# Optimization experiments

Measured on AMD Instinct MI355X. Metric: run time of the kernel, lower is better.

The kernel has to match this reference:

```python
import jax, jax.numpy as jnp
import numpy as np
from jax import lax

B, C, W, H = 4, 64, 128, 128
K = 9            # snake kernel length
OC = 64          # out channels
EXTEND_SCOPE = 1.0
EPS = 1e-5
DN = ('NCHW', 'OIHW', 'NCHW')


def setup_inputs() -> dict:
    key = jax.random.key(0)
    ks = jax.random.split(key, 4)
    f = jax.random.normal(ks[0], (B, C, W, H), jnp.float32)
    offset_w = jax.random.normal(ks[1], (2 * K, C, 3, 3), jnp.float32) * 0.05
    offset_b = jnp.zeros((2 * K,), jnp.float32)
    bn_gamma = jnp.ones((2 * K,), jnp.float32)
    bn_beta = jnp.zeros((2 * K,), jnp.float32)
    bn_mean = jnp.zeros((2 * K,), jnp.float32)
    bn_var = jnp.ones((2 * K,), jnp.float32)
    conv_w = jax.random.normal(ks[2], (OC, C, K, 1), jnp.float32) * 0.05
    conv_b = jnp.zeros((OC,), jnp.float32)
    gn_gamma = jnp.ones((OC,), jnp.float32)
    gn_beta = jnp.zeros((OC,), jnp.float32)
    return dict(f=f, offset_w=offset_w, offset_b=offset_b, bn_gamma=bn_gamma,
                bn_beta=bn_beta, bn_mean=bn_mean, bn_var=bn_var,
                conv_w=conv_w, conv_b=conv_b, gn_gamma=gn_gamma, gn_beta=gn_beta)


def _dsconv(f, offset_w, offset_b, bn_gamma, bn_beta, bn_mean, bn_var,
            conv_w, conv_b, gn_gamma, gn_beta):
    # 1) offset branch: 3x3 conv -> BN (eval) -> tanh
    off = lax.conv_general_dilated(f, offset_w, (1, 1), 'SAME', dimension_numbers=DN)
    off = off + offset_b[None, :, None, None]
    off = (off - bn_mean[None, :, None, None]) * lax.rsqrt(bn_var + EPS)[None, :, None, None]
    off = off * bn_gamma[None, :, None, None] + bn_beta[None, :, None, None]
    off = jnp.tanh(off)
    y_off = off[:, :K]                      # [B,K,W,H]  (morph==0 uses y offsets)

    # 2) cumulative offset recurrence outward from the kernel center.
    # NOTE: indices 0 and K-1 keep their raw (non-accumulated) offsets,
    # exactly reproducing the original loop `for i in range(1, center)`.
    c = K // 2
    offs = [y_off[:, k] for k in range(K)]  # each [B,W,H]
    new = list(offs)
    new[c] = jnp.zeros_like(offs[c])
    for i in range(1, c):
        new[c + i] = new[c + i - 1] + offs[c + i]
        new[c - i] = new[c - i + 1] + offs[c - i]
    y_cum = jnp.stack(new, axis=1)          # [B,K,W,H]

    # 3) sampling coordinates (morph==0): y = row index + accumulated offset,
    # x = col index + linspace(-K//2, K//2, K) (python floor-div semantics).
    lin = jnp.linspace((-K) // 2, K // 2, K).astype(f.dtype)      # [-5..4] for K=9
    y = jnp.arange(W, dtype=f.dtype)[None, None, :, None] + y_cum * EXTEND_SCOPE
    x = jnp.broadcast_to(jnp.arange(H, dtype=f.dtype)[None, None, None, :]
                         + lin[None, :, None, None], (B, K, W, H))
    # layout [B, K*W, H] with row index = w*K + k
    ys = jnp.transpose(y, (0, 2, 1, 3)).reshape(B, K * W, H)
    xs = jnp.transpose(x, (0, 2, 1, 3)).reshape(B, K * W, H)

    # 4) bilinear gather from f (NCHW -> BWHC for channel-last gathers)
    y0 = jnp.clip(jnp.floor(ys).astype(jnp.int32), 0, W - 1)
    y1 = jnp.clip(y0 + 1, 0, W - 1)
    x0 = jnp.clip(jnp.floor(xs).astype(jnp.int32), 0, H - 1)
    x1 = jnp.clip(x0 + 1, 0, H - 1)
    fb = jnp.transpose(f, (0, 2, 3, 1))                  # [B,W,H,C]
    gather = jax.vmap(lambda fm, yy, xx: fm[yy, xx])     # -> [B,K*W,H,C]
    va0 = gather(fb, y0, x0)
    va1 = gather(fb, y0, x1)
    vb0 = gather(fb, y1, x0)
    vb1 = gather(fb, y1, x1)
    y0f, y1f = y0.astype(f.dtype), y1.astype(f.dtype)
    x0f, x1f = x0.astype(f.dtype), x1.astype(f.dtype)
    out = (va0 * ((y1f - ys) * (x1f - xs))[..., None]
           + va1 * ((y1f - ys) * (xs - x0f))[..., None]
           + vb0 * ((ys - y0f) * (x1f - xs))[..., None]
           + vb1 * ((ys - y0f) * (xs - x0f))[..., None])
    deformed = jnp.transpose(out, (0, 3, 1, 2))          # [B,C,K*W,H]

    # 5) (K,1)-strided conv collapses the K snake samples -> [B,OC,W,H]
    z = lax.conv_general_dilated(deformed, conv_w, (K, 1), 'VALID', dimension_numbers=DN)
    z = z + conv_b[None, :, None, None]

    # 6) GroupNorm(OC//4 groups) + ReLU
    G = OC // 4
    zg = z.reshape(B, G, OC // G, W, H)
    mu = zg.mean(axis=(2, 3, 4), keepdims=True)
    var = zg.var(axis=(2, 3, 4), keepdims=True)
    zg = (zg - mu) * lax.rsqrt(var + EPS)
    z = zg.reshape(B, OC, W, H) * gn_gamma[None, :, None, None] + gn_beta[None, :, None, None]
    return jax.nn.relu(z)


def reference(f, offset_w, offset_b, bn_gamma, bn_beta, bn_mean, bn_var,
              conv_w, conv_b, gn_gamma, gn_beta):
    return _dsconv(f, offset_w, offset_b, bn_gamma, bn_beta, bn_mean, bn_var,
                   conv_w, conv_b, gn_gamma, gn_beta)
```

## Files before the change

kernel.cpp:

```cpp
#include <hip/hip_runtime.h>
#include <hip/hip_bf16.h>

#define EPSV 1e-5f

typedef __attribute__((ext_vector_type(8))) short short8;
typedef __attribute__((ext_vector_type(4))) float f32x4;

__global__ __launch_bounds__(256) void k_transpose(const float* __restrict__ f,
                                                   ushort* __restrict__ fbh) {
    int blk = blockIdx.x;
    int xt  = blk & 1;
    int y   = (blk >> 1) & 127;
    int b   = blk >> 8;
    __shared__ float tile[64][65];
    int t  = threadIdx.x;
    int x  = t & 63;
    int c0 = t >> 6;
    const float* src = f + (((size_t)b * 64) * 128 + y) * 128 + xt * 64;
#pragma unroll
    for (int i = 0; i < 64; i += 4) {
        tile[c0 + i][x] = src[(size_t)(c0 + i) * (128 * 128) + x];
    }
    __syncthreads();
    ushort* dst = fbh + (((size_t)b * 128 + y) * 128 + xt * 64) * 64;
    int cc = t & 63;
    int x0 = t >> 6;
#pragma unroll
    for (int i = 0; i < 64; i += 4) {
        dst[(size_t)(x0 + i) * 64 + cc] =
            __bfloat16_as_ushort(__float2bfloat16(tile[cc][x0 + i]));
    }
}

__global__ __launch_bounds__(256) void k_prep(const float* __restrict__ cw,
                                              ushort* __restrict__ wpk,
                                              float* __restrict__ stats) {
    int idx = blockIdx.x * 256 + threadIdx.x;
    int j  = idx & 7;
    int l  = (idx >> 3) & 63;
    int ot = (idx >> 9) & 3;
    int kk = (idx >> 11) & 1;
    int k  = idx >> 12;
    int c  = kk * 32 + ((l >> 4) << 3) + j;
    int oc = (ot << 4) + (l & 15);
    float v = cw[((size_t)oc * 64 + c) * 9 + k];
    wpk[idx] = __bfloat16_as_ushort(__float2bfloat16(v));
    if (idx < 128) stats[idx] = 0.f;
}

__global__ __launch_bounds__(128) void k_off1(const float* __restrict__ f,
                                              const float* __restrict__ ow,
                                              float* __restrict__ offp) {
    int blk = blockIdx.x;
    int cq = blk & 3;
    int w  = (blk >> 2) & 127;
    int b  = blk >> 9;
    int c0 = cq << 4;
    __shared__ float wl[9 * 16 * 12];
    int t = threadIdx.x;
    for (int i = t; i < 9 * 16 * 9; i += 128) {
        int kc  = i / 9;
        int tap = i - kc * 9;
        int k   = kc >> 4;
        int ci  = kc & 15;
        wl[kc * 12 + tap] = ow[((size_t)(k * 64 + c0 + ci)) * 9 + tap];
    }
    __syncthreads();
    int h = t;
    float acc[9];
#pragma unroll
    for (int k = 0; k < 9; ++k) acc[k] = 0.f;
    const float* fbase = f + (((size_t)b * 64 + c0) << 14);
    for (int ci = 0; ci < 16; ++ci) {
        const float* fc = fbase + ((size_t)ci << 14);
        float v[9];
#pragma unroll
        for (int dy = 0; dy < 3; ++dy) {
            int yy = w + dy - 1;
            bool yok = (unsigned)yy < 128u;
#pragma unroll
            for (int dx = 0; dx < 3; ++dx) {
                int xx = h + dx - 1;
                v[dy * 3 + dx] = (yok && ((unsigned)xx < 128u)) ? fc[(yy << 7) + xx] : 0.f;
            }
        }
#pragma unroll
        for (int k = 0; k < 9; ++k) {
            const float* wp = &wl[(k * 16 + ci) * 12];
            float4 wa = *(const float4*)wp;
            float4 wb = *(const float4*)(wp + 4);
            acc[k] += v[0] * wa.x + v[1] * wa.y + v[2] * wa.z + v[3] * wa.w
                    + v[4] * wb.x + v[5] * wb.y + v[6] * wb.z + v[7] * wb.w
                    + v[8] * wp[8];
        }
    }
#pragma unroll
    for (int k = 0; k < 9; ++k)
        offp[(((size_t)cq * 36 + b * 9 + k) << 14) + (w << 7) + h] = acc[k];
}

__global__ __launch_bounds__(256) void k_off2(const float* __restrict__ offp,
                                              const float* __restrict__ ob,
                                              const float* __restrict__ bng,
                                              const float* __restrict__ bnb,
                                              const float* __restrict__ bnm,
                                              const float* __restrict__ bnv,
                                              float* __restrict__ yc) {
    int idx = blockIdx.x * 256 + threadIdx.x;
    int b = idx >> 14;
    int rest = idx & 16383;
    int w = rest >> 7;
    float tk[9];
#pragma unroll
    for (int k = 0; k < 9; ++k) {
        int o = ((b * 9 + k) << 14) + rest;
        float zz = offp[o] + offp[o + 589824] + offp[o + 2 * 589824] + offp[o + 3 * 589824];
        zz += ob[k];
        zz = (zz - bnm[k]) * rsqrtf(bnv[k] + EPSV);
        zz = zz * bng[k] + bnb[k];
        tk[k] = tanhf(zz);
    }
    float nw_[9];
    nw_[4] = 0.f;
    nw_[5] = tk[5];
    nw_[6] = nw_[5] + tk[6];
    nw_[7] = nw_[6] + tk[7];
    nw_[8] = tk[8];
    nw_[3] = tk[3];
    nw_[2] = nw_[3] + tk[2];
    nw_[1] = nw_[2] + tk[1];
    nw_[0] = tk[0];
#pragma unroll
    for (int k = 0; k < 9; ++k)
        yc[((b * 9 + k) << 14) + rest] = (float)w + nw_[k];
}

__global__ __launch_bounds__(256) void k_main(
    const ushort* __restrict__ fbh, const float* __restrict__ yc,
    const ushort* __restrict__ wpk, const float* __restrict__ cb,
    float* __restrict__ z, float* __restrict__ stats)
{
    __shared__ union {
        struct {
            ushort A[32 * 64];
            float  tup[9][32][8];
        } p;
        float Z2[32 * 65];
    } sm;
    __shared__ float redS[16];
    __shared__ float redQ[16];

    int jb = blockIdx.x;
    int orig = (jb & 7) * 256 + (jb >> 3);
    int hq = orig & 3;
    int w  = (orig >> 2) & 127;
    int b  = orig >> 9;
    int t    = threadIdx.x;
    int lane = t & 63;
    int wid  = t >> 6;
    int m = wid & 1;
    int n = wid >> 1;

    for (int i = t; i < 288; i += 256) {
        int k  = i >> 5;
        int px = i & 31;
        int h  = (hq << 5) + px;
        float ys = yc[((b * 9 + k) << 14) + (w << 7) + h];
        float xs = (float)h + (-5.0f + 1.125f * (float)k);
        int y0 = min(max((int)floorf(ys), 0), 127);
        int y1 = min(y0 + 1, 127);
        int x0 = min(max((int)floorf(xs), 0), 127);
        int x1 = min(x0 + 1, 127);
        float wy0 = (float)y1 - ys, wy1 = ys - (float)y0;
        float wx0 = (float)x1 - xs, wx1 = xs - (float)x0;
        float* tp = sm.p.tup[k][px];
        tp[0] = __int_as_float(((((b << 7) + y0) << 7) + x0) << 7);
        tp[1] = __int_as_float(((((b << 7) + y0) << 7) + x1) << 7);
        tp[2] = __int_as_float(((((b << 7) + y1) << 7) + x0) << 7);
        tp[3] = __int_as_float(((((b << 7) + y1) << 7) + x1) << 7);
        tp[4] = wy0 * wx0;
        tp[5] = wy0 * wx1;
        tp[6] = wy1 * wx0;
        tp[7] = wy1 * wx1;
    }
    __syncthreads();

    f32x4 acc0 = {0.f, 0.f, 0.f, 0.f};
    f32x4 acc1 = {0.f, 0.f, 0.f, 0.f};
    const char* fp = (const char*)fbh;
    char* Ab = (char*)sm.p.A;
    int cg = t & 15;
    int pq = t >> 4;
    int cgo = cg << 3;
    const short8* wp8 = (const short8*)wpk;

    for (int k = 0; k < 9; ++k) {
        int fb0 = ((k * 2) * 4 + (n << 1)) * 64 + lane;
        short8 wf00 = wp8[fb0];
        short8 wf01 = wp8[fb0 + 64];
        short8 wf10 = wp8[fb0 + 256];
        short8 wf11 = wp8[fb0 + 320];

#pragma unroll
        for (int s = 0; s < 2; ++s) {
            int px = pq + (s << 4);
            const float* tp = sm.p.tup[k][px];
            float4 tr = *(const float4*)tp;
            float4 tw = *(const float4*)(tp + 4);
            uint2 u00 = *(const uint2*)(fp + __float_as_int(tr.x) + cgo);
            uint2 u01 = *(const uint2*)(fp + __float_as_int(tr.y) + cgo);
            uint2 u10 = *(const uint2*)(fp + __float_as_int(tr.z) + cgo);
            uint2 u11 = *(const uint2*)(fp + __float_as_int(tr.w) + cgo);
            float a0 = __uint_as_float(u00.x << 16) * tw.x + __uint_as_float(u01.x << 16) * tw.y
                     + __uint_as_float(u10.x << 16) * tw.z + __uint_as_float(u11.x << 16) * tw.w;
            float a1 = __uint_as_float(u00.x & 0xffff0000u) * tw.x + __uint_as_float(u01.x & 0xffff0000u) * tw.y
                     + __uint_as_float(u10.x & 0xffff0000u) * tw.z + __uint_as_float(u11.x & 0xffff0000u) * tw.w;
            float a2 = __uint_as_float(u00.y << 16) * tw.x + __uint_as_float(u01.y << 16) * tw.y
                     + __uint_as_float(u10.y << 16) * tw.z + __uint_as_float(u11.y << 16) * tw.w;
            float a3 = __uint_as_float(u00.y & 0xffff0000u) * tw.x + __uint_as_float(u01.y & 0xffff0000u) * tw.y
                     + __uint_as_float(u10.y & 0xffff0000u) * tw.z + __uint_as_float(u11.y & 0xffff0000u) * tw.w;
            uint2 pk;
            pk.x = (uint)__bfloat16_as_ushort(__float2bfloat16(a0))
                 | ((uint)__bfloat16_as_ushort(__float2bfloat16(a1)) << 16);
            pk.y = (uint)__bfloat16_as_ushort(__float2bfloat16(a2))
                 | ((uint)__bfloat16_as_ushort(__float2bfloat16(a3)) << 16);
            int wb = (px << 7) + (cgo ^ ((px & 7) << 4));
            *(uint2*)(Ab + wb) = pk;
        }
        __syncthreads();

        {
            int row = (m << 4) + (lane & 15);
            int rb0 = (row << 7) + ((((lane >> 4) << 4)) ^ ((lane & 7) << 4));
            short8 af0 = *(const short8*)(Ab + rb0);
            short8 af1 = *(const short8*)(Ab + (rb0 ^ 64));
            acc0 = __builtin_amdgcn_mfma_f32_16x16x32_bf16(af0, wf00, acc0, 0, 0, 0);
            acc0 = __builtin_amdgcn_mfma_f32_16x16x32_bf16(af1, wf10, acc0, 0, 0, 0);
            acc1 = __builtin_amdgcn_mfma_f32_16x16x32_bf16(af0, wf01, acc1, 0, 0, 0);
            acc1 = __builtin_amdgcn_mfma_f32_16x16x32_bf16(af1, wf11, acc1, 0, 0, 0);
        }
        __syncthreads();
    }

    int lane15 = lane & 15;
    float b0 = cb[(n << 5) + lane15];
    float b1 = cb[(n << 5) + 16 + lane15];
    float v00 = acc0.x + b0, v01 = acc0.y + b0, v02 = acc0.z + b0, v03 = acc0.w + b0;
    float v10 = acc1.x + b1, v11 = acc1.y + b1, v12 = acc1.z + b1, v13 = acc1.w + b1;
    float s0 = v00 + v01 + v02 + v03;
    float q0 = v00 * v00 + v01 * v01 + v02 * v02 + v03 * v03;
    float s1 = v10 + v11 + v12 + v13;
    float q1 = v10 * v10 + v11 * v11 + v12 * v12 + v13 * v13;
    if (t < 16) { redS[t] = 0.f; redQ[t] = 0.f; }
    __syncthreads();
    int g0 = (n << 3) + (lane15 >> 2);
    atomicAdd(&redS[g0], s0);     atomicAdd(&redQ[g0], q0);
    atomicAdd(&redS[g0 + 4], s1); atomicAdd(&redQ[g0 + 4], q1);
    int pxb = (m << 4) + ((lane >> 4) << 2);
    int ocb = (n << 5) + lane15;
    sm.Z2[(pxb + 0) * 65 + ocb] = v00;
    sm.Z2[(pxb + 1) * 65 + ocb] = v01;
    sm.Z2[(pxb + 2) * 65 + ocb] = v02;
    sm.Z2[(pxb + 3) * 65 + ocb] = v03;
    sm.Z2[(pxb + 0) * 65 + ocb + 16] = v10;
    sm.Z2[(pxb + 1) * 65 + ocb + 16] = v11;
    sm.Z2[(pxb + 2) * 65 + ocb + 16] = v12;
    sm.Z2[(pxb + 3) * 65 + ocb + 16] = v13;
    __syncthreads();
    if (t < 16) {
        atomicAdd(&stats[((size_t)b * 16 + t) * 2 + 0], redS[t]);
        atomicAdd(&stats[((size_t)b * 16 + t) * 2 + 1], redQ[t]);
    }
    int oc = t >> 2, part = t & 3;
    float4 o0, o1;
    o0.x = sm.Z2[(part * 8 + 0) * 65 + oc];
    o0.y = sm.Z2[(part * 8 + 1) * 65 + oc];
    o0.z = sm.Z2[(part * 8 + 2) * 65 + oc];
    o0.w = sm.Z2[(part * 8 + 3) * 65 + oc];
    o1.x = sm.Z2[(part * 8 + 4) * 65 + oc];
    o1.y = sm.Z2[(part * 8 + 5) * 65 + oc];
    o1.z = sm.Z2[(part * 8 + 6) * 65 + oc];
    o1.w = sm.Z2[(part * 8 + 7) * 65 + oc];
    float* zp = z + (((size_t)(b << 6) + oc) << 14) + (w << 7) + (hq << 5) + part * 8;
    *(float4*)zp = o0;
    *(float4*)(zp + 4) = o1;
}

__global__ __launch_bounds__(256) void k_gn(const float* __restrict__ z,
                                            const float* __restrict__ stats,
                                            const float* __restrict__ gg,
                                            const float* __restrict__ gb,
                                            float* __restrict__ out) {
    int idx = blockIdx.x * 256 + threadIdx.x;
    size_t base = (size_t)idx * 4;
    int oc = (int)((base >> 14) & 63);
    int b  = (int)(base >> 20);
    int g  = oc >> 2;
    float sm = stats[((size_t)b * 16 + g) * 2 + 0];
    float sq = stats[((size_t)b * 16 + g) * 2 + 1];
    const float cnt = 65536.f;
    float mu  = sm / cnt;
    float var = sq / cnt - mu * mu;
    float inv = rsqrtf(var + EPSV);
    float gam = gg[oc] * inv;
    float bet = gb[oc] - mu * gam;
    float4 v = *(const float4*)(z + base);
    v.x = fmaxf(v.x * gam + bet, 0.f);
    v.y = fmaxf(v.y * gam + bet, 0.f);
    v.z = fmaxf(v.z * gam + bet, 0.f);
    v.w = fmaxf(v.w * gam + bet, 0.f);
    *(float4*)(out + base) = v;
}

extern "C" void kernel_launch(void* const* d_in, const int* in_sizes, int n_in,
                              void* d_out, int out_size, void* d_ws, size_t ws_size,
                              hipStream_t stream) {
    const float* f   = (const float*)d_in[0];
    const float* ow  = (const float*)d_in[1];
    const float* ob  = (const float*)d_in[2];
    const float* bng = (const float*)d_in[3];
    const float* bnb = (const float*)d_in[4];
    const float* bnm = (const float*)d_in[5];
    const float* bnv = (const float*)d_in[6];
    const float* cw  = (const float*)d_in[7];
    const float* cb  = (const float*)d_in[8];
    const float* gg  = (const float*)d_in[9];
    const float* gb  = (const float*)d_in[10];

    char* wsb = (char*)d_ws;
    ushort* fbh = (ushort*)wsb;
    float*  yc  = (float*)(wsb + 8388608);
    ushort* wpk = (ushort*)(wsb + 10747904);
    float*  z   = (float*)(wsb + 10821632);
    float*  st  = (float*)(wsb + 27598848);
    float*  offp= (float*)(wsb + 27599360);

    k_prep<<<144, 256, 0, stream>>>(cw, wpk, st);
    k_transpose<<<1024, 256, 0, stream>>>(f, fbh);
    k_off1<<<2048, 128, 0, stream>>>(f, ow, offp);
    k_off2<<<256, 256, 0, stream>>>(offp, ob, bng, bnb, bnm, bnv, yc);
    k_main<<<2048, 256, 0, stream>>>(fbh, yc, wpk, cb, z, st);
    k_gn<<<4096, 256, 0, stream>>>(z, st, gg, gb, (float*)d_out);
}
```

Measured before the change: 179.7 us.

## Fuse offset conv into main kernel via split-bf16 MFMA and double-buffer gathers

Drops the separate FP32 offset convolution and offset-finalize kernels. The 3x3 offset conv now runs inside the main kernel as an implicit GEMM on MFMA, with a split hi/lo bf16 representation of both input and weights to keep roughly FP32 accuracy. The prep, transpose and weight-packing kernels are merged into one launch. The deformable-gather loop is software pipelined with double-buffered LDS so global gathers overlap the MFMAs. This cuts kernel launches and the offset intermediates' global traffic, at the cost of an extra lo-part feature map, more LDS per block, and offset work concentrated in two waves.

Measured after the change: 158.2 us. -12.0%, faster.

```diff
diff --git a/kernel.cpp b/kernel.cpp
--- a/kernel.cpp
+++ b/kernel.cpp
@@ -6,149 +6,100 @@
 typedef __attribute__((ext_vector_type(8))) short short8;
 typedef __attribute__((ext_vector_type(4))) float f32x4;
 
-__global__ __launch_bounds__(256) void k_transpose(const float* __restrict__ f,
-                                                   ushort* __restrict__ fbh) {
+__device__ __forceinline__ uint2 bilerp_pack(uint2 u00, uint2 u01, uint2 u10, uint2 u11, float4 tw) {
+    float a0 = __uint_as_float(u00.x << 16) * tw.x + __uint_as_float(u01.x << 16) * tw.y
+             + __uint_as_float(u10.x << 16) * tw.z + __uint_as_float(u11.x << 16) * tw.w;
+    float a1 = __uint_as_float(u00.x & 0xffff0000u) * tw.x + __uint_as_float(u01.x & 0xffff0000u) * tw.y
+             + __uint_as_float(u10.x & 0xffff0000u) * tw.z + __uint_as_float(u11.x & 0xffff0000u) * tw.w;
+    float a2 = __uint_as_float(u00.y << 16) * tw.x + __uint_as_float(u01.y << 16) * tw.y
+             + __uint_as_float(u10.y << 16) * tw.z + __uint_as_float(u11.y << 16) * tw.w;
+    float a3 = __uint_as_float(u00.y & 0xffff0000u) * tw.x + __uint_as_float(u01.y & 0xffff0000u) * tw.y
+             + __uint_as_float(u10.y & 0xffff0000u) * tw.z + __uint_as_float(u11.y & 0xffff0000u) * tw.w;
+    uint2 pk;
+    pk.x = (uint)__bfloat16_as_ushort(__float2bfloat16(a0))
+         | ((uint)__bfloat16_as_ushort(__float2bfloat16(a1)) << 16);
+    pk.y = (uint)__bfloat16_as_ushort(__float2bfloat16(a2))
+         | ((uint)__bfloat16_as_ushort(__float2bfloat16(a3)) << 16);
+    return pk;
+}
+
+__global__ __launch_bounds__(256) void k_pre(const float* __restrict__ f,
+                                             const float* __restrict__ cw,
+                                             const float* __restrict__ ow,
+                                             ushort* __restrict__ fbh,
+                                             ushort* __restrict__ flo,
+                                             ushort* __restrict__ wpk,
+                                             ushort* __restrict__ wpk2,
+                                             float* __restrict__ stats) {
     int blk = blockIdx.x;
-    int xt  = blk & 1;
-    int y   = (blk >> 1) & 127;
-    int b   = blk >> 8;
-    __shared__ float tile[64][65];
-    int t  = threadIdx.x;
-    int x  = t & 63;
-    int c0 = t >> 6;
-    const float* src = f + (((size_t)b * 64) * 128 + y) * 128 + xt * 64;
-#pragma unroll
-    for (int i = 0; i < 64; i += 4) {
-        tile[c0 + i][x] = src[(size_t)(c0 + i) * (128 * 128) + x];
-    }
-    __syncthreads();
-    ushort* dst = fbh + (((size_t)b * 128 + y) * 128 + xt * 64) * 64;
-    int cc = t & 63;
-    int x0 = t >> 6;
-#pragma unroll
-    for (int i = 0; i < 64; i += 4) {
-        dst[(size_t)(x0 + i) * 64 + cc] =
-            __bfloat16_as_ushort(__float2bfloat16(tile[cc][x0 + i]));
+    int t = threadIdx.x;
+    if (blk < 1024) {
+        __shared__ float tile[64][65];
+        int xt = blk & 1;
+        int y  = (blk >> 1) & 127;
+        int b  = blk >> 8;
+        int x = t & 63, c0 = t >> 6;
+        const float* src = f + (((size_t)b * 64) * 128 + y) * 128 + xt * 64;
+#pragma unroll
+        for (int i = 0; i < 64; i += 4)
+            tile[c0 + i][x] = src[(size_t)(c0 + i) * 16384 + x];
+        __syncthreads();
+        size_t dbase = (((size_t)b * 128 + y) * 128 + xt * 64) * 64;
+        int cc = t & 63, x0 = t >> 6;
+#pragma unroll
+        for (int i = 0; i < 64; i += 4) {
+            float v = tile[cc][x0 + i];
+            ushort hi = __bfloat16_as_ushort(__float2bfloat16(v));
+            float vhi = __uint_as_float((uint)hi << 16);
+            ushort lo = __bfloat16_as_ushort(__float2bfloat16(v - vhi));
+            fbh[dbase + (size_t)(x0 + i) * 64 + cc] = hi;
+            flo[dbase + (size_t)(x0 + i) * 64 + cc] = lo;
+        }
+    } else if (blk < 1168) {
+        int idx = (blk - 1024) * 256 + t;
+        int j  = idx & 7;
+        int l  = (idx >> 3) & 63;
+        int ot = (idx >> 9) & 3;
+        int kk = (idx >> 11) & 1;
+        int k  = idx >> 12;
+        int c  = kk * 32 + ((l >> 4) << 3) + j;
+        int oc = (ot << 4) + (l & 15);
+        wpk[idx] = __bfloat16_as_ushort(__float2bfloat16(cw[((size_t)oc * 64 + c) * 9 + k]));
+        if (idx < 128) stats[idx] = 0.f;
+    } else {
+        int idx = (blk - 1168) * 256 + t;
+        int j   = idx & 7;
+        int l   = (idx >> 3) & 63;
+        int kk  = (idx >> 9) & 1;
+        int tap = idx >> 10;
+        int c   = kk * 32 + ((l >> 4) << 3) + j;
+        int n   = l & 15;
+        float v = (n < 9) ? ow[((size_t)n * 64 + c) * 9 + tap] : 0.f;
+        ushort hi = __bfloat16_as_ushort(__float2bfloat16(v));
+        float vhi = __uint_as_float((uint)hi << 16);
+        ushort lo = __bfloat16_as_ushort(__float2bfloat16(v - vhi));
+        wpk2[idx] = hi;
+        wpk2[idx + 9216] = lo;
     }
 }
 
-__global__ __launch_bounds__(256) void k_prep(const float* __restrict__ cw,
-                                              ushort* __restrict__ wpk,
-                                              float* __restrict__ stats) {
-    int idx = blockIdx.x * 256 + threadIdx.x;
-    int j  = idx & 7;
-    int l  = (idx >> 3) & 63;
-    int ot = (idx >> 9) & 3;
-    int kk = (idx >> 11) & 1;
-    int k  = idx >> 12;
-    int c  = kk * 32 + ((l >> 4) << 3) + j;
-    int oc = (ot << 4) + (l & 15);
-    float v = cw[((size_t)oc * 64 + c) * 9 + k];
-    wpk[idx] = __bfloat16_as_ushort(__float2bfloat16(v));
-    if (idx < 128) stats[idx] = 0.f;
-}
-
-__global__ __launch_bounds__(128) void k_off1(const float* __restrict__ f,
-                                              const float* __restrict__ ow,
-                                              float* __restrict__ offp) {
-    int blk = blockIdx.x;
-    int cq = blk & 3;
-    int w  = (blk >> 2) & 127;
-    int b  = blk >> 9;
-    int c0 = cq << 4;
-    __shared__ float wl[9 * 16 * 12];
-    int t = threadIdx.x;
-    for (int i = t; i < 9 * 16 * 9; i += 128) {
-        int kc  = i / 9;
-        int tap = i - kc * 9;
-        int k   = kc >> 4;
-        int ci  = kc & 15;
-        wl[kc * 12 + tap] = ow[((size_t)(k * 64 + c0 + ci)) * 9 + tap];
-    }
-    __syncthreads();
-    int h = t;
-    float acc[9];
-#pragma unroll
-    for (int k = 0; k < 9; ++k) acc[k] = 0.f;
-    const float* fbase = f + (((size_t)b * 64 + c0) << 14);
-    for (int ci = 0; ci < 16; ++ci) {
-        const float* fc = fbase + ((size_t)ci << 14);
-        float v[9];
-#pragma unroll
-        for (int dy = 0; dy < 3; ++dy) {
-            int yy = w + dy - 1;
-            bool yok = (unsigned)yy < 128u;
-#pragma unroll
-            for (int dx = 0; dx < 3; ++dx) {
-                int xx = h + dx - 1;
-                v[dy * 3 + dx] = (yok && ((unsigned)xx < 128u)) ? fc[(yy << 7) + xx] : 0.f;
-            }
-        }
-#pragma unroll
-        for (int k = 0; k < 9; ++k) {
-            const float* wp = &wl[(k * 16 + ci) * 12];
-            float4 wa = *(const float4*)wp;
-            float4 wb = *(const float4*)(wp + 4);
-            acc[k] += v[0] * wa.x + v[1] * wa.y + v[2] * wa.z + v[3] * wa.w
-                    + v[4] * wb.x + v[5] * wb.y + v[6] * wb.z + v[7] * wb.w
-                    + v[8] * wp[8];
-        }
-    }
-#pragma unroll
-    for (int k = 0; k < 9; ++k)
-        offp[(((size_t)cq * 36 + b * 9 + k) << 14) + (w << 7) + h] = acc[k];
-}
-
-__global__ __launch_bounds__(256) void k_off2(const float* __restrict__ offp,
-                                              const float* __restrict__ ob,
-                                              const float* __restrict__ bng,
-                                              const float* __restrict__ bnb,
-                                              const float* __restrict__ bnm,
-                                              const float* __restrict__ bnv,
-                                              float* __restrict__ yc) {
-    int idx = blockIdx.x * 256 + threadIdx.x;
-    int b = idx >> 14;
-    int rest = idx & 16383;
-    int w = rest >> 7;
-    float tk[9];
-#pragma unroll
-    for (int k = 0; k < 9; ++k) {
-        int o = ((b * 9 + k) << 14) + rest;
-        float zz = offp[o] + offp[o + 589824] + offp[o + 2 * 589824] + offp[o + 3 * 589824];
-        zz += ob[k];
-        zz = (zz - bnm[k]) * rsqrtf(bnv[k] + EPSV);
-        zz = zz * bng[k] + bnb[k];
-        tk[k] = tanhf(zz);
-    }
-    float nw_[9];
-    nw_[4] = 0.f;
-    nw_[5] = tk[5];
-    nw_[6] = nw_[5] + tk[6];
-    nw_[7] = nw_[6] + tk[7];
-    nw_[8] = tk[8];
-    nw_[3] = tk[3];
-    nw_[2] = nw_[3] + tk[2];
-    nw_[1] = nw_[2] + tk[1];
-    nw_[0] = tk[0];
-#pragma unroll
-    for (int k = 0; k < 9; ++k)
-        yc[((b * 9 + k) << 14) + rest] = (float)w + nw_[k];
-}
-
-__global__ __launch_bounds__(256) void k_main(
-    const ushort* __restrict__ fbh, const float* __restrict__ yc,
-    const ushort* __restrict__ wpk, const float* __restrict__ cb,
+__global__ __launch_bounds__(256) void k_fused(
+    const ushort* __restrict__ fbh,
+    const ushort* __restrict__ flo,
+    const ushort* __restrict__ wpk,
+    const ushort* __restrict__ wpk2,
+    const float* __restrict__ ob, const float* __restrict__ bng,
+    const float* __restrict__ bnb, const float* __restrict__ bnm,
+    const float* __restrict__ bnv, const float* __restrict__ cb,
     float* __restrict__ z, float* __restrict__ stats)
 {
-    __shared__ union {
-        struct {
-            ushort A[32 * 64];
-            float  tup[9][32][8];
-        } p;
-        float Z2[32 * 65];
-    } sm;
-    __shared__ float redS[16];
-    __shared__ float redQ[16];
+    __shared__ struct {
+        ushort AH[2][2048];
+        ushort AL[2][2048];
+        float  tup[9][32][8];
+        float  cs[32][12];
+    } smx;
+    __shared__ float redS[16], redQ[16];
 
     int jb = blockIdx.x;
     int orig = (jb & 7) * 256 + (jb >> 3);
@@ -161,87 +112,203 @@
     int m = wid & 1;
     int n = wid >> 1;
 
-    for (int i = t; i < 288; i += 256) {
-        int k  = i >> 5;
-        int px = i & 31;
-        int h  = (hq << 5) + px;
-        float ys = yc[((b * 9 + k) << 14) + (w << 7) + h];
-        float xs = (float)h + (-5.0f + 1.125f * (float)k);
-        int y0 = min(max((int)floorf(ys), 0), 127);
-        int y1 = min(y0 + 1, 127);
-        int x0 = min(max((int)floorf(xs), 0), 127);
-        int x1 = min(x0 + 1, 127);
-        float wy0 = (float)y1 - ys, wy1 = ys - (float)y0;
-        float wx0 = (float)x1 - xs, wx1 = xs - (float)x0;
-        float* tp = sm.p.tup[k][px];
-        tp[0] = __int_as_float(((((b << 7) + y0) << 7) + x0) << 7);
-        tp[1] = __int_as_float(((((b << 7) + y0) << 7) + x1) << 7);
-        tp[2] = __int_as_float(((((b << 7) + y1) << 7) + x0) << 7);
-        tp[3] = __int_as_float(((((b << 7) + y1) << 7) + x1) << 7);
-        tp[4] = wy0 * wx0;
-        tp[5] = wy0 * wx1;
-        tp[6] = wy1 * wx0;
-        tp[7] = wy1 * wx1;
+    const char* fpH = (const char*)fbh;
+    const char* fpL = (const char*)flo;
+    int cg  = t & 15;
+    int pq  = t >> 4;
+    int cgo = cg << 3;
+
+    int frow = (m << 4) + (lane & 15);
+    int frb0 = (frow << 7) + (((lane >> 4) << 4) ^ ((lane & 7) << 4));
+
+    f32x4 acc0k = {0.f, 0.f, 0.f, 0.f};
+    const short8* wp2 = (const short8*)wpk2;
+
+    {
+        int ysrc = w - 1;
+        bool rok = (unsigned)ysrc < 128u;
+        char* AbH = (char*)smx.AH[0];
+        char* AbL = (char*)smx.AL[0];
+#pragma unroll
+        for (int s = 0; s < 2; ++s) {
+            int px = pq + (s << 4);
+            int xsrc = (hq << 5) + px - 1;
+            uint2 vh = make_uint2(0u, 0u), vl = make_uint2(0u, 0u);
+            if (rok && ((unsigned)xsrc < 128u)) {
+                int off = ((((((b << 7) + ysrc) << 7) + xsrc)) << 7) + cgo;
+                vh = *(const uint2*)(fpH + off);
+                vl = *(const uint2*)(fpL + off);
+            }
+            int wb = (px << 7) + (cgo ^ ((px & 7) << 4));
+            *(uint2*)(AbH + wb) = vh;
+            *(uint2*)(AbL + wb) = vl;
+        }
+    }
+    for (int tap = 0; tap < 9; ++tap) {
+        __syncthreads();
+        int cur = tap & 1;
+        uint2 gh[2] = {make_uint2(0u, 0u), make_uint2(0u, 0u)};
+        uint2 gl[2] = {make_uint2(0u, 0u), make_uint2(0u, 0u)};
+        if (tap < 8) {
+            int tn = tap + 1;
+            int dy = tn / 3;
+            int dx = tn - dy * 3;
+            int ysrc = w + dy - 1;
+            bool rok = (unsigned)ysrc < 128u;
+#pragma unroll
+            for (int s = 0; s < 2; ++s) {
+                int px = pq + (s << 4);
+                int xsrc = (hq << 5) + px + dx - 1;
+                if (rok && ((unsigned)xsrc < 128u)) {
+                    int off = ((((((b << 7) + ysrc) << 7) + xsrc)) << 7) + cgo;
+                    gh[s] = *(const uint2*)(fpH + off);
+                    gl[s] = *(const uint2*)(fpL + off);
+                }
+            }
+        }
+        if (wid < 2) {
+            const char* ArH = (const char*)smx.AH[cur];
+            const char* ArL = (const char*)smx.AL[cur];
+            short8 ah0 = *(const short8*)(ArH + frb0);
+            short8 ah1 = *(const short8*)(ArH + (frb0 ^ 64));
+            short8 al0 = *(const short8*)(ArL + frb0);
+            short8 al1 = *(const short8*)(ArL + (frb0 ^ 64));
+            short8 wh0 = wp2[(tap * 2 + 0) * 64 + lane];
+            short8 wh1 = wp2[(tap * 2 + 1) * 64 + lane];
+            short8 wl0 = wp2[1152 + (tap * 2 + 0) * 64 + lane];
+            short8 wl1 = wp2[1152 + (tap * 2 + 1) * 64 + lane];
+            acc0k = __builtin_amdgcn_mfma_f32_16x16x32_bf16(ah0, wh0, acc0k, 0, 0, 0);
+            acc0k = __builtin_amdgcn_mfma_f32_16x16x32_bf16(al0, wh0, acc0k, 0, 0, 0);
+            acc0k = __builtin_amdgcn_mfma_f32_16x16x32_bf16(ah0, wl0, acc0k, 0, 0, 0);
+            acc0k = __builtin_amdgcn_mfma_f32_16x16x32_bf16(ah1, wh1, acc0k, 0, 0, 0);
+            acc0k = __builtin_amdgcn_mfma_f32_16x16x32_bf16(al1, wh1, acc0k, 0, 0, 0);
+            acc0k = __builtin_amdgcn_mfma_f32_16x16x32_bf16(ah1, wl1, acc0k, 0, 0, 0);
+        }
+        if (tap < 8) {
+            char* AbH = (char*)smx.AH[cur ^ 1];
+            char* AbL = (char*)smx.AL[cur ^ 1];
+#pragma unroll
+            for (int s = 0; s < 2; ++s) {
+                int px = pq + (s << 4);
+                int wb = (px << 7) + (cgo ^ ((px & 7) << 4));
+                *(uint2*)(AbH + wb) = gh[s];
+                *(uint2*)(AbL + wb) = gl[s];
+            }
+        }
+    }
+    if (wid < 2) {
+#pragma unroll
+        for (int r = 0; r < 4; ++r) {
+            int pxo = (m << 4) + ((lane >> 4) << 2) + r;
+            int ko = lane & 15;
+            if (ko < 9) smx.cs[pxo][ko] = acc0k[r];
+        }
+    }
+    __syncthreads();
+    if (t < 32) {
+        float tk[9];
+#pragma unroll
+        for (int k = 0; k < 9; ++k) {
+            float zz = smx.cs[t][k] + ob[k];
+            zz = (zz - bnm[k]) * rsqrtf(bnv[k] + EPSV);
+            zz = zz * bng[k] + bnb[k];
+            tk[k] = tanhf(zz);
+        }
+        float nw_[9];
+        nw_[4] = 0.f;
+        nw_[5] = tk[5];
+        nw_[6] = nw_[5] + tk[6];
+        nw_[7] = nw_[6] + tk[7];
+        nw_[8] = tk[8];
+        nw_[3] = tk[3];
+        nw_[2] = nw_[3] + tk[2];
+        nw_[1] = nw_[2] + tk[1];
+        nw_[0] = tk[0];
+        int h = (hq << 5) + t;
+#pragma unroll
+        for (int k = 0; k < 9; ++k) {
+            float ys = (float)w + nw_[k];
+            float xs = (float)h + (-5.0f + 1.125f * (float)k);
+            int y0 = min(max((int)floorf(ys), 0), 127);
+            int y1 = min(y0 + 1, 127);
+            int x0 = min(max((int)floorf(xs), 0), 127);
+            int x1 = min(x0 + 1, 127);
+            float wy0 = (float)y1 - ys, wy1 = ys - (float)y0;
+            float wx0 = (float)x1 - xs, wx1 = xs - (float)x0;
+            float* tp = smx.tup[k][t];
+            tp[0] = __int_as_float(((((b << 7) + y0) << 7) + x0) << 7);
+            tp[1] = __int_as_float(((((b << 7) + y0) << 7) + x1) << 7);
+            tp[2] = __int_as_float(((((b << 7) + y1) << 7) + x0) << 7);
+            tp[3] = __int_as_float(((((b << 7) + y1) << 7) + x1) << 7);
+            tp[4] = wy0 * wx0;
+            tp[5] = wy0 * wx1;
+            tp[6] = wy1 * wx0;
+            tp[7] = wy1 * wx1;
+        }
     }
     __syncthreads();
 
     f32x4 acc0 = {0.f, 0.f, 0.f, 0.f};
     f32x4 acc1 = {0.f, 0.f, 0.f, 0.f};
-    const char* fp = (const char*)fbh;
-    char* Ab = (char*)sm.p.A;
-    int cg = t & 15;
-    int pq = t >> 4;
-    int cgo = cg << 3;
     const short8* wp8 = (const short8*)wpk;
 
+    {
+        char* Ab = (char*)smx.AH[0];
+#pragma unroll
+        for (int s = 0; s < 2; ++s) {
+            int px = pq + (s << 4);
+            const float* tp = smx.tup[0][px];
+            float4 tr = *(const float4*)tp;
+            float4 tw = *(const float4*)(tp + 4);
+            uint2 u00 = *(const uint2*)(fpH + __float_as_int(tr.x) + cgo);
+            uint2 u01 = *(const uint2*)(fpH + __float_as_int(tr.y) + cgo);
+            uint2 u10 = *(const uint2*)(fpH + __float_as_int(tr.z) + cgo);
+            uint2 u11 = *(const uint2*)(fpH + __float_as_int(tr.w) + cgo);
+            *(uint2*)(Ab + (px << 7) + (cgo ^ ((px & 7) << 4))) = bilerp_pack(u00, u01, u10, u11, tw);
+        }
+    }
     for (int k = 0; k < 9; ++k) {
-        int fb0 = ((k * 2) * 4 + (n << 1)) * 64 + lane;
+        __syncthreads();
+        int cur = k & 1;
+        uint2 u[2][4];
+        float4 twn[2];
+        if (k < 8) {
+#pragma unroll
+            for (int s = 0; s < 2; ++s) {
+                int px = pq + (s << 4);
+                const float* tp = smx.tup[k + 1][px];
+                float4 tr = *(const float4*)tp;
+                twn[s] = *(const float4*)(tp + 4);
+                u[s][0] = *(const uint2*)(fpH + __float_as_int(tr.x) + cgo);
+                u[s][1] = *(const uint2*)(fpH + __float_as_int(tr.y) + cgo);
+                u[s][2] = *(const uint2*)(fpH + __float_as_int(tr.z) + cgo);
+                u[s][3] = *(const uint2*)(fpH + __float_as_int(tr.w) + cgo);
+            }
+        }
+        int fb0 = (k * 8 + (n << 1)) * 64 + lane;
         short8 wf00 = wp8[fb0];
         short8 wf01 = wp8[fb0 + 64];
         short8 wf10 = wp8[fb0 + 256];
         short8 wf11 = wp8[fb0 + 320];
-
-#pragma unroll
-        for (int s = 0; s < 2; ++s) {
-            int px = pq + (s << 4);
-            const float* tp = sm.p.tup[k][px];
-            float4 tr = *(const float4*)tp;
-            float4 tw = *(const float4*)(tp + 4);
-            uint2 u00 = *(const uint2*)(fp + __float_as_int(tr.x) + cgo);
-            uint2 u01 = *(const uint2*)(fp + __float_as_int(tr.y) + cgo);
-            uint2 u10 = *(const uint2*)(fp + __float_as_int(tr.z) + cgo);
-            uint2 u11 = *(const uint2*)(fp + __float_as_int(tr.w) + cgo);
-            float a0 = __uint_as_float(u00.x << 16) * tw.x + __uint_as_float(u01.x << 16) * tw.y
-                     + __uint_as_float(u10.x << 16) * tw.z + __uint_as_float(u11.x << 16) * tw.w;
-            float a1 = __uint_as_float(u00.x & 0xffff0000u) * tw.x + __uint_as_float(u01.x & 0xffff0000u) * tw.y
-                     + __uint_as_float(u10.x & 0xffff0000u) * tw.z + __uint_as_float(u11.x & 0xffff0000u) * tw.w;
-            float a2 = __uint_as_float(u00.y << 16) * tw.x + __uint_as_float(u01.y << 16) * tw.y
-                     + __uint_as_float(u10.y << 16) * tw.z + __uint_as_float(u11.y << 16) * tw.w;
-            float a3 = __uint_as_float(u00.y & 0xffff0000u) * tw.x + __uint_as_float(u01.y & 0xffff0000u) * tw.y
-                     + __uint_as_float(u10.y & 0xffff0000u) * tw.z + __uint_as_float(u11.y & 0xffff0000u) * tw.w;
-            uint2 pk;
-            pk.x = (uint)__bfloat16_as_ushort(__float2bfloat16(a0))
-                 | ((uint)__bfloat16_as_ushort(__float2bfloat16(a1)) << 16);
-            pk.y = (uint)__bfloat16_as_ushort(__float2bfloat16(a2))
-                 | ((uint)__bfloat16_as_ushort(__float2bfloat16(a3)) << 16);
-            int wb = (px << 7) + (cgo ^ ((px & 7) << 4));
-            *(uint2*)(Ab + wb) = pk;
-        }
-        __syncthreads();
-
-        {
-            int row = (m << 4) + (lane & 15);
-            int rb0 = (row << 7) + ((((lane >> 4) << 4)) ^ ((lane & 7) << 4));
-            short8 af0 = *(const short8*)(Ab + rb0);
-            short8 af1 = *(const short8*)(Ab + (rb0 ^ 64));
-            acc0 = __builtin_amdgcn_mfma_f32_16x16x32_bf16(af0, wf00, acc0, 0, 0, 0);
-            acc0 = __builtin_amdgcn_mfma_f32_16x16x32_bf16(af1, wf10, acc0, 0, 0, 0);
-            acc1 = __builtin_amdgcn_mfma_f32_16x16x32_bf16(af0, wf01, acc1, 0, 0, 0);
-            acc1 = __builtin_amdgcn_mfma_f32_16x16x32_bf16(af1, wf11, acc1, 0, 0, 0);
-        }
-        __syncthreads();
-    }
-
+        const char* Ar = (const char*)smx.AH[cur];
+        short8 af0 = *(const short8*)(Ar + frb0);
+        short8 af1 = *(const short8*)(Ar + (frb0 ^ 64));
+        acc0 = __builtin_amdgcn_mfma_f32_16x16x32_bf16(af0, wf00, acc0, 0, 0, 0);
+        acc0 = __builtin_amdgcn_mfma_f32_16x16x32_bf16(af1, wf10, acc0, 0, 0, 0);
+        acc1 = __builtin_amdgcn_mfma_f32_16x16x32_bf16(af0, wf01, acc1, 0, 0, 0);
+        acc1 = __builtin_amdgcn_mfma_f32_16x16x32_bf16(af1, wf11, acc1, 0, 0, 0);
+        if (k < 8) {
+            char* Ab = (char*)smx.AH[cur ^ 1];
+#pragma unroll
+            for (int s = 0; s < 2; ++s) {
+                int px = pq + (s << 4);
+                *(uint2*)(Ab + (px << 7) + (cgo ^ ((px & 7) << 4))) =
+                    bilerp_pack(u[s][0], u[s][1], u[s][2], u[s][3], twn[s]);
+            }
+        }
+    }
+
+    float* Z2 = (float*)&smx;
     int lane15 = lane & 15;
     float b0 = cb[(n << 5) + lane15];
     float b1 = cb[(n << 5) + 16 + lane15];
@@ -258,14 +325,14 @@
     atomicAdd(&redS[g0 + 4], s1); atomicAdd(&redQ[g0 + 4], q1);
     int pxb = (m << 4) + ((lane >> 4) << 2);
     int ocb = (n << 5) + lane15;
-    sm.Z2[(pxb + 0) * 65 + ocb] = v00;
-    sm.Z2[(pxb + 1) * 65 + ocb] = v01;
-    sm.Z2[(pxb + 2) * 65 + ocb] = v02;
-    sm.Z2[(pxb + 3) * 65 + ocb] = v03;
-    sm.Z2[(pxb + 0) * 65 + ocb + 16] = v10;
-    sm.Z2[(pxb + 1) * 65 + ocb + 16] = v11;
-    sm.Z2[(pxb + 2) * 65 + ocb + 16] = v12;
-    sm.Z2[(pxb + 3) * 65 + ocb + 16] = v13;
+    Z2[(pxb + 0) * 65 + ocb] = v00;
+    Z2[(pxb + 1) * 65 + ocb] = v01;
+    Z2[(pxb + 2) * 65 + ocb] = v02;
+    Z2[(pxb + 3) * 65 + ocb] = v03;
+    Z2[(pxb + 0) * 65 + ocb + 16] = v10;
+    Z2[(pxb + 1) * 65 + ocb + 16] = v11;
+    Z2[(pxb + 2) * 65 + ocb + 16] = v12;
+    Z2[(pxb + 3) * 65 + ocb + 16] = v13;
     __syncthreads();
     if (t < 16) {
         atomicAdd(&stats[((size_t)b * 16 + t) * 2 + 0], redS[t]);
@@ -273,14 +340,14 @@
     }
     int oc = t >> 2, part = t & 3;
     float4 o0, o1;
-    o0.x = sm.Z2[(part * 8 + 0) * 65 + oc];
-    o0.y = sm.Z2[(part * 8 + 1) * 65 + oc];
-    o0.z = sm.Z2[(part * 8 + 2) * 65 + oc];
-    o0.w = sm.Z2[(part * 8 + 3) * 65 + oc];
-    o1.x = sm.Z2[(part * 8 + 4) * 65 + oc];
-    o1.y = sm.Z2[(part * 8 + 5) * 65 + oc];
-    o1.z = sm.Z2[(part * 8 + 6) * 65 + oc];
-    o1.w = sm.Z2[(part * 8 + 7) * 65 + oc];
+    o0.x = Z2[(part * 8 + 0) * 65 + oc];
+    o0.y = Z2[(part * 8 + 1) * 65 + oc];
+    o0.z = Z2[(part * 8 + 2) * 65 + oc];
+    o0.w = Z2[(part * 8 + 3) * 65 + oc];
+    o1.x = Z2[(part * 8 + 4) * 65 + oc];
+    o1.y = Z2[(part * 8 + 5) * 65 + oc];
+    o1.z = Z2[(part * 8 + 6) * 65 + oc];
+    o1.w = Z2[(part * 8 + 7) * 65 + oc];
     float* zp = z + (((size_t)(b << 6) + oc) << 14) + (w << 7) + (hq << 5) + part * 8;
     *(float4*)zp = o0;
     *(float4*)(zp + 4) = o1;
@@ -328,17 +395,14 @@
     const float* gb  = (const float*)d_in[10];
 
     char* wsb = (char*)d_ws;
-    ushort* fbh = (ushort*)wsb;
-    float*  yc  = (float*)(wsb + 8388608);
-    ushort* wpk = (ushort*)(wsb + 10747904);
-    float*  z   = (float*)(wsb + 10821632);
-    float*  st  = (float*)(wsb + 27598848);
-    float*  offp= (float*)(wsb + 27599360);
-
-    k_prep<<<144, 256, 0, stream>>>(cw, wpk, st);
-    k_transpose<<<1024, 256, 0, stream>>>(f, fbh);
-    k_off1<<<2048, 128, 0, stream>>>(f, ow, offp);
-    k_off2<<<256, 256, 0, stream>>>(offp, ob, bng, bnb, bnm, bnv, yc);
-    k_main<<<2048, 256, 0, stream>>>(fbh, yc, wpk, cb, z, st);
+    ushort* fbh  = (ushort*)wsb;
+    ushort* flo  = (ushort*)(wsb + 8388608);
+    ushort* wpk  = (ushort*)(wsb + 16777216);
+    ushort* wpk2 = (ushort*)(wsb + 16850944);
+    float*  z    = (float*)(wsb + 16887808);
+    float*  st   = (float*)(wsb + 33665024);
+
+    k_pre<<<1204, 256, 0, stream>>>(f, cw, ow, fbh, flo, wpk, wpk2, st);
+    k_fused<<<2048, 256, 0, stream>>>(fbh, flo, wpk, wpk2, ob, bng, bnb, bnm, bnv, cb, z, st);
     k_gn<<<4096, 256, 0, stream>>>(z, st, gg, gb, (float*)d_out);
 }
```
